# Optimization experiments

Hardware: AMD Instinct MI355X
Metric: run time of the kernel (lower is better)

## Reference

```python
import jax, jax.numpy as jnp
import numpy as np
import math

N_TOKEN = (56, 135, 18, 87, 18, 25)
EMB_SIZES = (128, 256, 64, 512, 128, 128)
D_MODEL = 512; N_LAYER = 12; N_HEAD = 8; D_HEAD = 64; D_FF = 2048
B = 2; S = 512
EPS_ATTN = 1e-6; EPS_LN = 1e-5


def _pos_encoding(seq, d):
    pos = jnp.arange(seq, dtype=jnp.float32)[:, None]
    div = jnp.exp(jnp.arange(0, d, 2, dtype=jnp.float32) * (-math.log(10000.0) / d))
    pe = jnp.zeros((seq, d), dtype=jnp.float32)
    pe = pe.at[:, 0::2].set(jnp.sin(pos * div))
    pe = pe.at[:, 1::2].set(jnp.cos(pos * div))
    return pe


def _ln(x, g, b):
    m = x.mean(-1, keepdims=True)
    v = ((x - m) ** 2).mean(-1, keepdims=True)
    return (x - m) * jax.lax.rsqrt(v + EPS_LN) * g + b


def setup_inputs():
    key = jax.random.key(0)
    ks = iter(jax.random.split(key, 128))
    def w(shape, s=0.02):
        return jax.random.normal(next(ks), shape, dtype=jnp.float32) * s
    inp = {}
    inp["x"] = jax.random.randint(next(ks), (B, S, 6), 0, min(N_TOKEN)).astype(jnp.int32)
    emb_names = ["emb_tempo", "emb_chord", "emb_barbeat", "emb_pitch", "emb_duration", "emb_velocity"]
    for n, v, e in zip(emb_names, N_TOKEN, EMB_SIZES):
        inp[n] = w((v, e), 1.0)
    inp["in_w"] = w((sum(EMB_SIZES), D_MODEL)); inp["in_b"] = jnp.zeros((D_MODEL,), jnp.float32)
    L = N_LAYER
    for nm, shp in [("Wq", (L, D_MODEL, D_MODEL)), ("Wk", (L, D_MODEL, D_MODEL)), ("Wv", (L, D_MODEL, D_MODEL)), ("Wo", (L, D_MODEL, D_MODEL)), ("W1", (L, D_MODEL, D_FF)), ("W2", (L, D_FF, D_MODEL))]:
        inp[nm] = w(shp)
    for nm, shp in [("bq", (L, D_MODEL)), ("bk", (L, D_MODEL)), ("bv", (L, D_MODEL)), ("bo", (L, D_MODEL)), ("bf1", (L, D_FF)), ("bf2", (L, D_MODEL)), ("b1n", (L, D_MODEL)), ("b2n", (L, D_MODEL))]:
        inp[nm] = jnp.zeros(shp, jnp.float32)
    inp["g1"] = jnp.ones((L, D_MODEL), jnp.float32); inp["g2"] = jnp.ones((L, D_MODEL), jnp.float32)
    inp["gf"] = jnp.ones((D_MODEL,), jnp.float32); inp["bfn"] = jnp.zeros((D_MODEL,), jnp.float32)
    for i, v in enumerate(N_TOKEN):
        inp[f"pw{i}"] = w((D_MODEL, v)); inp[f"pb{i}"] = jnp.zeros((v,), jnp.float32)
        inp[f"vw{i}"] = w((v, 1)); inp[f"vb{i}"] = jnp.zeros((1,), jnp.float32)
    return inp


def _layer(h, p):
    (wq, bq_, wk, bk_, wv, bv_, wo, bo_, g1_, b1_, g2_, b2_, w1, bf1_, w2, bf2_) = p
    # causal-linear attention (fast-transformers), feature map elu(x)+1
    q = (h @ wq + bq_).reshape(B, S, N_HEAD, D_HEAD)
    k = (h @ wk + bk_).reshape(B, S, N_HEAD, D_HEAD)
    v = (h @ wv + bv_).reshape(B, S, N_HEAD, D_HEAD)
    Q = jax.nn.elu(q) + 1.0
    K = jax.nn.elu(k) + 1.0
    kv = jnp.cumsum(jnp.einsum('bshd,bshm->bshdm', K, v), axis=1)  # causal prefix KV state
    num = jnp.einsum('bshd,bshdm->bshm', Q, kv)
    z = 1.0 / (jnp.einsum('bshd,bshd->bsh', Q, jnp.cumsum(K, axis=1)) + EPS_ATTN)
    a = (num * z[..., None]).reshape(B, S, D_MODEL) @ wo + bo_
    # fast-transformers TransformerEncoderLayer: post-norm residuals, exact GELU FFN
    h2 = _ln(h + a, g1_, b1_)
    y = jax.nn.gelu(h2 @ w1 + bf1_, approximate=False) @ w2 + bf2_
    return _ln(h2 + y, g2_, b2_), None


def reference(x, emb_tempo, emb_chord, emb_barbeat, emb_pitch, emb_duration, emb_velocity, in_w, in_b, Wq, bq, Wk, bk, Wv, bv, Wo, bo, g1, b1n, g2, b2n, W1, bf1, W2, bf2, gf, bfn, pw0, pb0, vw0, vb0, pw1, pb1, vw1, vb1, pw2, pb2, vw2, vb2, pw3, pb3, vw3, vb3, pw4, pb4, vw4, vb4, pw5, pb5, vw5, vb5):
    tables = [emb_tempo, emb_chord, emb_barbeat, emb_pitch, emb_duration, emb_velocity]
    embs = [tables[i][x[..., i]] * math.sqrt(EMB_SIZES[i]) for i in range(6)]
    h = jnp.concatenate(embs, axis=-1) @ in_w + in_b
    h = h + _pos_encoding(S, D_MODEL)
    h, _ = jax.lax.scan(jax.checkpoint(_layer), h, (Wq, bq, Wk, bk, Wv, bv, Wo, bo, g1, b1n, g2, b2n, W1, bf1, W2, bf2))
    h = _ln(h, gf, bfn)
    heads = [(pw0, pb0, vw0, vb0), (pw1, pb1, vw1, vb1), (pw2, pb2, vw2, vb2), (pw3, pb3, vw3, vb3), (pw4, pb4, vw4, vb4), (pw5, pb5, vw5, vb5)]
    total = 0.0
    for pw, pb, vw, vb in heads:
        total = total + jnp.mean((h @ pw + pb) @ vw + vb, axis=1)  # [B,1]
    return total / 6.0
```

## Files before the change

kernel.cpp:

```cpp
#include <hip/hip_runtime.h>
#include <math.h>

typedef _Float16 f16;
typedef _Float16 f16x8 __attribute__((ext_vector_type(8)));
typedef float f32x4 __attribute__((ext_vector_type(4)));

#define TOK 1024
#define DM  512
#define SEQ 512
#define NB  2
#define CHUNK 32
#define NCH (SEQ/CHUNK)

__global__ __launch_bounds__(256) void embed_gather(
    const int* __restrict__ x,
    const float* __restrict__ t0, const float* __restrict__ t1,
    const float* __restrict__ t2, const float* __restrict__ t3,
    const float* __restrict__ t4, const float* __restrict__ t5,
    f16* __restrict__ E) {
  int t = blockIdx.x;
  int tid = threadIdx.x;
  const int* xb = x + t * 6;
  for (int c = tid; c < 1216; c += 256) {
    float val;
    if (c < 128)       val = t0[xb[0]*128 + c]        * 11.313708498984761f;
    else if (c < 384)  val = t1[xb[1]*256 + (c-128)]  * 16.0f;
    else if (c < 448)  val = t2[xb[2]*64  + (c-384)]  * 8.0f;
    else if (c < 960)  val = t3[xb[3]*512 + (c-448)]  * 22.627416997969522f;
    else if (c < 1088) val = t4[xb[4]*128 + (c-960)]  * 11.313708498984761f;
    else               val = t5[xb[5]*128 + (c-1088)] * 11.313708498984761f;
    E[(size_t)t*1216 + c] = (f16)val;
  }
}

__global__ __launch_bounds__(256) void transp_convert(
    const float* __restrict__ in, f16* __restrict__ out,
    int K, int N, size_t instride, size_t outstride) {
  int lz = blockIdx.z;
  const float* I = in + (size_t)lz * instride;
  f16* O = out + (size_t)lz * outstride;
  __shared__ float tile[32][33];
  int k0 = blockIdx.x * 32, n0 = blockIdx.y * 32;
  int tid = threadIdx.x;
  int cr = tid >> 5, cc = tid & 31;
#pragma unroll
  for (int p = 0; p < 4; ++p)
    tile[cr + p*8][cc] = I[(size_t)(k0 + cr + p*8) * N + n0 + cc];
  __syncthreads();
#pragma unroll
  for (int p = 0; p < 4; ++p)
    O[(size_t)(n0 + cr + p*8) * K + k0 + cc] = (f16)tile[cc][cr + p*8];
}

__global__ __launch_bounds__(256) void transp_convert_qkvo(
    const float* __restrict__ Wq, const float* __restrict__ Wk,
    const float* __restrict__ Wv, const float* __restrict__ Wo,
    f16* __restrict__ qkvw, f16* __restrict__ wot) {
  int z = blockIdx.z;
  int lz = z >> 2, m = z & 3;
  const float* I = ((m == 0) ? Wq : (m == 1) ? Wk : (m == 2) ? Wv : Wo)
                   + (size_t)lz * 262144;
  f16* O = (m < 3) ? qkvw + (size_t)lz * 786432 + (size_t)m * 262144
                   : wot + (size_t)lz * 262144;
  __shared__ float tile[32][33];
  int k0 = blockIdx.x * 32, n0 = blockIdx.y * 32;
  int tid = threadIdx.x;
  int cr = tid >> 5, cc = tid & 31;
#pragma unroll
  for (int p = 0; p < 4; ++p)
    tile[cr + p*8][cc] = I[(size_t)(k0 + cr + p*8) * 512 + n0 + cc];
  __syncthreads();
#pragma unroll
  for (int p = 0; p < 4; ++p)
    O[(size_t)(n0 + cr + p*8) * 512 + k0 + cc] = (f16)tile[cc][cr + p*8];
}

template<int E>
__global__ __launch_bounds__(256) void mfma_gemm(
    const f16* __restrict__ A, const f16* __restrict__ Bt,
    const float* __restrict__ b0, const float* __restrict__ b1,
    const float* __restrict__ b2,
    float* __restrict__ o0, float* __restrict__ o1, float* __restrict__ o2,
    int M, int K, int N) {
  __shared__ f16 As[64][72];
  __shared__ f16 Bs[64][72];
  const int tid = threadIdx.x;
  const int m0 = blockIdx.x * 64, n0 = blockIdx.y * 64;
  const int w = tid >> 6, l = tid & 63;
  const int wr = w >> 1, wc = w & 1;
  const int g = l >> 4, r = l & 15;
  const int lr = tid >> 2, lc = (tid & 3) * 8;
  f32x4 acc[2][2] = {};
  const f16* Ap = A + (size_t)(m0 + lr) * K + lc;
  const f16* Bp = Bt + (size_t)(n0 + lr) * K + lc;
  for (int k0 = 0; k0 < K; k0 += 64) {
    *(f16x8*)&As[lr][lc]      = *(const f16x8*)(Ap + k0);
    *(f16x8*)&As[lr][lc + 32] = *(const f16x8*)(Ap + k0 + 32);
    *(f16x8*)&Bs[lr][lc]      = *(const f16x8*)(Bp + k0);
    *(f16x8*)&Bs[lr][lc + 32] = *(const f16x8*)(Bp + k0 + 32);
    __syncthreads();
#pragma unroll
    for (int kk = 0; kk < 2; ++kk) {
      f16x8 a0  = *(const f16x8*)&As[wr*32 + r][kk*32 + g*8];
      f16x8 a1  = *(const f16x8*)&As[wr*32 + 16 + r][kk*32 + g*8];
      f16x8 bv0 = *(const f16x8*)&Bs[wc*32 + r][kk*32 + g*8];
      f16x8 bv1 = *(const f16x8*)&Bs[wc*32 + 16 + r][kk*32 + g*8];
      acc[0][0] = __builtin_amdgcn_mfma_f32_16x16x32_f16(a0, bv0, acc[0][0], 0, 0, 0);
      acc[0][1] = __builtin_amdgcn_mfma_f32_16x16x32_f16(a0, bv1, acc[0][1], 0, 0, 0);
      acc[1][0] = __builtin_amdgcn_mfma_f32_16x16x32_f16(a1, bv0, acc[1][0], 0, 0, 0);
      acc[1][1] = __builtin_amdgcn_mfma_f32_16x16x32_f16(a1, bv1, acc[1][1], 0, 0, 0);
    }
    __syncthreads();
  }
#pragma unroll
  for (int m = 0; m < 2; ++m) {
    int row = m0 + wr*32 + m*16 + g*4;
#pragma unroll
    for (int n = 0; n < 2; ++n) {
      int col = n0 + wc*32 + n*16 + r;
      float pediv = 0.0f;
      if (E == 3) pediv = __expf((float)(col >> 1) * (-0.035977892070386504f));
#pragma unroll
      for (int i = 0; i < 4; ++i) {
        float v = acc[m][n][i];
        if (E == 2) {
          int which = col >> 9;
          int lc2 = col & 511;
          const float* bb = (which == 0) ? b0 : (which == 1) ? b1 : b2;
          float* oo = (which == 0) ? o0 : (which == 1) ? o1 : o2;
          v += bb[lc2];
          if (which < 2) v = (v > 0.0f) ? v + 1.0f : __expf(v);
          oo[(size_t)(row + i) * 512 + lc2] = v;
        } else if (E == 1) {
          v += b0[col];
          v = 0.5f * v * (1.0f + erff(v * 0.70710678118654752f));
          ((f16*)o0)[(size_t)(row + i) * N + col] = (f16)v;
        } else if (E == 3) {
          v += b0[col];
          float ang = (float)((row + i) & (SEQ-1)) * pediv;
          v += (col & 1) ? cosf(ang) : sinf(ang);
          o0[(size_t)(row + i) * N + col] = v;
          ((f16*)o1)[(size_t)(row + i) * N + col] = (f16)v;
        } else {
          v += b0[col];
          o0[(size_t)(row + i) * N + col] = v;
        }
      }
    }
  }
}

__global__ __launch_bounds__(256) void attn_chunk_sums(
    const float* __restrict__ Kg, const float* __restrict__ Vg,
    float* __restrict__ kvst, float* __restrict__ ksum) {
  int ch = blockIdx.x, bh = blockIdx.y;
  int b = bh >> 3, h = bh & 7;
  __shared__ float Ks[CHUNK][65], Vs[CHUNK][65];
  int tid = threadIdx.x;
  const float* Kbase = Kg + ((size_t)(b*SEQ + ch*CHUNK))*DM + h*64;
  const float* Vbase = Vg + ((size_t)(b*SEQ + ch*CHUNK))*DM + h*64;
#pragma unroll
  for (int l = 0; l < CHUNK*64/256; ++l) {
    int e = tid + l*256;
    int r = e >> 6, c = e & 63;
    Ks[r][c] = Kbase[(size_t)r*DM + c];
    Vs[r][c] = Vbase[(size_t)r*DM + c];
  }
  __syncthreads();
  int d = tid >> 2, m0 = (tid & 3) * 16;
  float acc[16] = {};
  for (int s = 0; s < CHUNK; ++s) {
    float kd = Ks[s][d];
#pragma unroll
    for (int j = 0; j < 16; ++j) acc[j] += kd * Vs[s][m0+j];
  }
  float* dst = kvst + (((size_t)(bh*NCH + ch)*64 + d)*64) + m0;
#pragma unroll
  for (int j4 = 0; j4 < 4; ++j4)
    *(float4*)(dst + j4*4) = make_float4(acc[j4*4], acc[j4*4+1], acc[j4*4+2], acc[j4*4+3]);
  if (tid < 64) {
    float s = 0;
    for (int r = 0; r < CHUNK; ++r) s += Ks[r][tid];
    ksum[(size_t)(bh*NCH + ch)*64 + tid] = s;
  }
}

__global__ __launch_bounds__(256) void attn_scan_par(
    float* __restrict__ kvst, float* __restrict__ ksum) {
  int slice = blockIdx.x;
  int bh = blockIdx.y;
  int tid = threadIdx.x;
  if (slice < 16) {
    size_t base = (size_t)bh*NCH*4096 + slice*256 + tid;
    float run = 0.0f;
    for (int ch = 0; ch < NCH; ++ch) {
      size_t idx = base + (size_t)ch*4096;
      float t = kvst[idx];
      kvst[idx] = run;
      run += t;
    }
  } else if (tid < 64) {
    size_t base = (size_t)bh*NCH*64 + tid;
    float run = 0.0f;
    for (int ch = 0; ch < NCH; ++ch) {
      size_t idx = base + (size_t)ch*64;
      float t = ksum[idx];
      ksum[idx] = run;
      run += t;
    }
  }
}

__global__ __launch_bounds__(256) void attn_chunk_out(
    const float* __restrict__ Qg, const float* __restrict__ Kg,
    const float* __restrict__ Vg, const float* __restrict__ kvst,
    const float* __restrict__ ksum, f16* __restrict__ O) {
  int ch = blockIdx.x, bh = blockIdx.y;
  int b = bh >> 3, h = bh & 7;
  __shared__ float Qs[CHUNK][65], Ks[CHUNK][65], Vs[CHUNK][65];
  __shared__ float kvp[64][65];
  __shared__ float Sl[CHUNK][CHUNK+1];
  __shared__ float ksp[64];
  __shared__ float den[CHUNK];
  int tid = threadIdx.x;
  const float* Qbase = Qg + ((size_t)(b*SEQ + ch*CHUNK))*DM + h*64;
  const float* Kbase = Kg + ((size_t)(b*SEQ + ch*CHUNK))*DM + h*64;
  const float* Vbase = Vg + ((size_t)(b*SEQ + ch*CHUNK))*DM + h*64;
#pragma unroll
  for (int ld = 0; ld < CHUNK*64/256; ++ld) {
    int e = tid + ld*256;
    int rr = e >> 6, cc = e & 63;
    Qs[rr][cc] = Qbase[(size_t)rr*DM + cc];
    Ks[rr][cc] = Kbase[(size_t)rr*DM + cc];
    Vs[rr][cc] = Vbase[(size_t)rr*DM + cc];
  }
  {
    const float* src = kvst + (size_t)(bh*NCH + ch)*4096;
#pragma unroll
    for (int ld = 0; ld < 16; ++ld) {
      int e = tid + ld*256;
      kvp[e >> 6][e & 63] = src[e];
    }
  }
  if (tid < 64) ksp[tid] = ksum[(size_t)(bh*NCH + ch)*64 + tid];
  __syncthreads();
#pragma unroll
  for (int ld = 0; ld < 4; ++ld) {
    int e = tid + ld*256;
    int i = e >> 5, j = e & 31;
    float s = 0;
    for (int d2 = 0; d2 < 64; ++d2) s += Qs[i][d2] * Ks[j][d2];
    Sl[i][j] = s;
  }
  __syncthreads();
  if (tid < CHUNK) {
    int i = tid;
    float dsum = 0;
    for (int d2 = 0; d2 < 64; ++d2) dsum += Qs[i][d2] * ksp[d2];
    for (int j = 0; j <= i; ++j) dsum += Sl[i][j];
    den[i] = 1.0f / (dsum + 1e-6f);
  }
  __syncthreads();
  int row = tid >> 3, m0 = (tid & 7) * 8;
  float acc[8] = {};
  for (int d2 = 0; d2 < 64; ++d2) {
    float qd = Qs[row][d2];
#pragma unroll
    for (int j = 0; j < 8; ++j) acc[j] += qd * kvp[d2][m0+j];
  }
  for (int j2 = 0; j2 <= row; ++j2) {
    float sv = Sl[row][j2];
#pragma unroll
    for (int j = 0; j < 8; ++j) acc[j] += sv * Vs[j2][m0+j];
  }
  float zi = den[row];
  f16* dst = O + ((size_t)(b*SEQ + ch*CHUNK + row))*DM + h*64 + m0;
#pragma unroll
  for (int j = 0; j < 8; ++j) dst[j] = (f16)(acc[j] * zi);
}

__global__ __launch_bounds__(256) void resid_ln(
    const float* __restrict__ x, const float* __restrict__ r,
    const float* __restrict__ g, const float* __restrict__ bb,
    float* __restrict__ out, f16* __restrict__ out16) {
  int t = blockIdx.x;
  int tid = threadIdx.x;
  __shared__ float red[256];
  const float* xb = x + (size_t)t*DM;
  float v0 = xb[tid];
  float v1 = xb[tid+256];
  if (r) {
    const float* rb = r + (size_t)t*DM;
    v0 += rb[tid];
    v1 += rb[tid+256];
  }
  red[tid] = v0 + v1;
  __syncthreads();
  for (int o = 128; o > 0; o >>= 1) {
    if (tid < o) red[tid] += red[tid+o];
    __syncthreads();
  }
  float mean = red[0] * (1.0f/512.0f);
  __syncthreads();
  float d0 = v0 - mean, d1 = v1 - mean;
  red[tid] = d0*d0 + d1*d1;
  __syncthreads();
  for (int o = 128; o > 0; o >>= 1) {
    if (tid < o) red[tid] += red[tid+o];
    __syncthreads();
  }
  float rs = rsqrtf(red[0] * (1.0f/512.0f) + 1e-5f);
  float r0 = d0*rs*g[tid]     + bb[tid];
  float r1 = d1*rs*g[tid+256] + bb[tid+256];
  out[(size_t)t*DM + tid]     = r0;
  out[(size_t)t*DM + tid+256] = r1;
  if (out16) {
    out16[(size_t)t*DM + tid]     = (f16)r0;
    out16[(size_t)t*DM + tid+256] = (f16)r1;
  }
}

struct HeadPtrs {
  const float* pw[6]; const float* pb[6];
  const float* vw[6]; const float* vb[6];
};

__global__ __launch_bounds__(64) void head_u_par(HeadPtrs hp, float* __restrict__ U,
                                                 float* __restrict__ Cc) {
  const int vsz[6] = {56, 135, 18, 87, 18, 25};
  const int off[6] = {0, 56, 191, 209, 296, 314};
  int d = blockIdx.x;
  int tid = threadIdx.x;
  float acc = 0.0f;
  for (int jj = tid; jj < 339; jj += 64) {
    int i;
    if (jj < 191) i = (jj < 56) ? 0 : 1;
    else if (jj < 296) i = (jj < 209) ? 2 : 3;
    else i = (jj < 314) ? 4 : 5;
    int j = jj - off[i];
    float wv = (d < 512) ? hp.pw[i][(size_t)d * vsz[i] + j] : hp.pb[i][j];
    acc += wv * hp.vw[i][j];
  }
#pragma unroll
  for (int s = 32; s > 0; s >>= 1) acc += __shfl_down(acc, s);
  if (tid == 0) {
    if (d < 512) U[d] = acc;
    else {
      for (int i = 0; i < 6; ++i) acc += hp.vb[i][0];
      Cc[0] = acc;
    }
  }
}

__global__ __launch_bounds__(512) void final_out(
    const float* __restrict__ hf, const float* __restrict__ U,
    const float* __restrict__ Cc, float* __restrict__ out) {
  int b = blockIdx.x;
  int d = threadIdx.x;
  __shared__ float red[512];
  float cs = 0;
  const float* hb = hf + (size_t)b*SEQ*DM + d;
  for (int s = 0; s < SEQ; ++s) cs += hb[(size_t)s*DM];
  red[d] = cs * U[d];
  __syncthreads();
  for (int o = 256; o > 0; o >>= 1) {
    if (d < o) red[d] += red[d+o];
    __syncthreads();
  }
  if (d == 0) out[b] = (red[0] * (1.0f/512.0f) + Cc[0]) * (1.0f/6.0f);
}

extern "C" void kernel_launch(void* const* d_in, const int* in_sizes, int n_in,
                              void* d_out, int out_size, void* d_ws, size_t ws_size,
                              hipStream_t stream) {
  const int*   x    = (const int*)d_in[0];
  const float* T0   = (const float*)d_in[1];
  const float* T1   = (const float*)d_in[2];
  const float* T2   = (const float*)d_in[3];
  const float* T3   = (const float*)d_in[4];
  const float* T4   = (const float*)d_in[5];
  const float* T5   = (const float*)d_in[6];
  const float* in_w = (const float*)d_in[7];
  const float* in_b = (const float*)d_in[8];
  const float* Wq   = (const float*)d_in[9];
  const float* Wk   = (const float*)d_in[10];
  const float* Wv   = (const float*)d_in[11];
  const float* Wo   = (const float*)d_in[12];
  const float* W1   = (const float*)d_in[13];
  const float* W2   = (const float*)d_in[14];
  const float* bq   = (const float*)d_in[15];
  const float* bk   = (const float*)d_in[16];
  const float* bv   = (const float*)d_in[17];
  const float* bo   = (const float*)d_in[18];
  const float* bf1  = (const float*)d_in[19];
  const float* bf2  = (const float*)d_in[20];
  const float* b1n  = (const float*)d_in[21];
  const float* b2n  = (const float*)d_in[22];
  const float* g1   = (const float*)d_in[23];
  const float* g2   = (const float*)d_in[24];
  const float* gf   = (const float*)d_in[25];
  const float* bfn  = (const float*)d_in[26];
  HeadPtrs hp;
  for (int i = 0; i < 6; ++i) {
    hp.pw[i] = (const float*)d_in[27 + i*4];
    hp.pb[i] = (const float*)d_in[28 + i*4];
    hp.vw[i] = (const float*)d_in[29 + i*4];
    hp.vb[i] = (const float*)d_in[30 + i*4];
  }

  float* ws   = (float*)d_ws;
  float* h    = ws;
  float* q    = h    + 524288;
  float* k    = q    + 524288;
  float* v    = k    + 524288;
  float* a2   = v    + 524288;
  float* h2   = a2   + 524288;
  float* y    = h2   + 524288;
  float* kvst = y    + 524288;
  float* ksum = kvst + 1048576;
  float* U    = ksum + 16384;
  float* Cc   = U    + 512;
  f16* E16    = (f16*)(Cc + 16);
  f16* hf16   = E16   + 1245184;
  f16* h2f16  = hf16  + 524288;
  f16* attn16 = h2f16 + 524288;
  f16* ff16   = attn16+ 524288;
  f16* in_wt  = ff16  + 2097152;
  f16* qkvw   = in_wt + 623616;
  f16* wot    = qkvw  + 9437184;
  f16* w1t    = wot   + 3145728;
  f16* w2t    = w1t   + 12582912;

  transp_convert<<<dim3(38,16,1),  256, 0, stream>>>(in_w, in_wt, 1216, 512, 0, 0);
  transp_convert_qkvo<<<dim3(16,16,48), 256, 0, stream>>>(Wq, Wk, Wv, Wo, qkvw, wot);
  transp_convert<<<dim3(16,64,12), 256, 0, stream>>>(W1, w1t,  512, 2048, 1048576, 1048576);
  transp_convert<<<dim3(64,16,12), 256, 0, stream>>>(W2, w2t, 2048,  512, 1048576, 1048576);

  embed_gather<<<TOK, 256, 0, stream>>>(x, T0, T1, T2, T3, T4, T5, E16);
  mfma_gemm<3><<<dim3(16,8), 256, 0, stream>>>(E16, in_wt, in_b, nullptr, nullptr,
                                               h, (float*)hf16, nullptr, TOK, 1216, 512);

  for (int l = 0; l < 12; ++l) {
    mfma_gemm<2><<<dim3(16,24), 256, 0, stream>>>(hf16, qkvw + (size_t)l*786432,
        bq + l*512, bk + l*512, bv + l*512, q, k, v, TOK, 512, 1536);
    attn_chunk_sums<<<dim3(NCH,16), 256, 0, stream>>>(k, v, kvst, ksum);
    attn_scan_par<<<dim3(17,16), 256, 0, stream>>>(kvst, ksum);
    attn_chunk_out<<<dim3(NCH,16), 256, 0, stream>>>(q, k, v, kvst, ksum, attn16);
    mfma_gemm<0><<<dim3(16,8), 256, 0, stream>>>(attn16, wot + (size_t)l*262144,
        bo + l*512, nullptr, nullptr, a2, nullptr, nullptr, TOK, 512, 512);
    resid_ln<<<TOK, 256, 0, stream>>>(h, a2, g1 + l*512, b1n + l*512, h2, h2f16);
    mfma_gemm<1><<<dim3(16,32), 256, 0, stream>>>(h2f16, w1t + (size_t)l*1048576,
        bf1 + l*2048, nullptr, nullptr, (float*)ff16, nullptr, nullptr, TOK, 512, 2048);
    mfma_gemm<0><<<dim3(16,8), 256, 0, stream>>>(ff16, w2t + (size_t)l*1048576,
        bf2 + l*512, nullptr, nullptr, y, nullptr, nullptr, TOK, 2048, 512);
    resid_ln<<<TOK, 256, 0, stream>>>(h2, y, g2 + l*512, b2n + l*512, h, hf16);
  }

  resid_ln<<<TOK, 256, 0, stream>>>(h, nullptr, gf, bfn, h2, nullptr);
  head_u_par<<<513, 64, 0, stream>>>(hp, U, Cc);
  final_out<<<NB, 512, 0, stream>>>(h2, U, Cc, (float*)d_out);
}
```

Baseline: 1.524 ms.

## Split-K the N=512 GEMMs and reduce partials inside the residual LayerNorm

The output-projection and FFN down-projection GEMMs (N=512, only 128 blocks) now use a split-K kernel that launches 2 and 4 K-slices respectively, writing fp32 partials. The residual LayerNorm kernel sums those partials and adds the bias, fusing the split-K reduction and bias into an existing pass. This is meant to raise GPU occupancy on the small-grid GEMMs, at the cost of extra partial-buffer writes and reads to global memory.

```diff
diff --git a/kernel.cpp b/kernel.cpp
--- a/kernel.cpp
+++ b/kernel.cpp
@@ -141,11 +141,56 @@
           v += (col & 1) ? cosf(ang) : sinf(ang);
           o0[(size_t)(row + i) * N + col] = v;
           ((f16*)o1)[(size_t)(row + i) * N + col] = (f16)v;
-        } else {
-          v += b0[col];
-          o0[(size_t)(row + i) * N + col] = v;
         }
       }
+    }
+  }
+}
+
+__global__ __launch_bounds__(256) void mfma_gemm_sk(
+    const f16* __restrict__ A, const f16* __restrict__ Bt,
+    float* __restrict__ P, int M, int K, int N, int KS) {
+  __shared__ f16 As[64][72];
+  __shared__ f16 Bs[64][72];
+  const int tid = threadIdx.x;
+  const int m0 = blockIdx.x * 64, n0 = blockIdx.y * 64;
+  const int z = blockIdx.z;
+  const int w = tid >> 6, l = tid & 63;
+  const int wr = w >> 1, wc = w & 1;
+  const int g = l >> 4, r = l & 15;
+  const int lr = tid >> 2, lc = (tid & 3) * 8;
+  f32x4 acc[2][2] = {};
+  const f16* Ap = A + (size_t)(m0 + lr) * K + z*KS + lc;
+  const f16* Bp = Bt + (size_t)(n0 + lr) * K + z*KS + lc;
+  for (int k0 = 0; k0 < KS; k0 += 64) {
+    *(f16x8*)&As[lr][lc]      = *(const f16x8*)(Ap + k0);
+    *(f16x8*)&As[lr][lc + 32] = *(const f16x8*)(Ap + k0 + 32);
+    *(f16x8*)&Bs[lr][lc]      = *(const f16x8*)(Bp + k0);
+    *(f16x8*)&Bs[lr][lc + 32] = *(const f16x8*)(Bp + k0 + 32);
+    __syncthreads();
+#pragma unroll
+    for (int kk = 0; kk < 2; ++kk) {
+      f16x8 a0  = *(const f16x8*)&As[wr*32 + r][kk*32 + g*8];
+      f16x8 a1  = *(const f16x8*)&As[wr*32 + 16 + r][kk*32 + g*8];
+      f16x8 bv0 = *(const f16x8*)&Bs[wc*32 + r][kk*32 + g*8];
+      f16x8 bv1 = *(const f16x8*)&Bs[wc*32 + 16 + r][kk*32 + g*8];
+      acc[0][0] = __builtin_amdgcn_mfma_f32_16x16x32_f16(a0, bv0, acc[0][0], 0, 0, 0);
+      acc[0][1] = __builtin_amdgcn_mfma_f32_16x16x32_f16(a0, bv1, acc[0][1], 0, 0, 0);
+      acc[1][0] = __builtin_amdgcn_mfma_f32_16x16x32_f16(a1, bv0, acc[1][0], 0, 0, 0);
+      acc[1][1] = __builtin_amdgcn_mfma_f32_16x16x32_f16(a1, bv1, acc[1][1], 0, 0, 0);
+    }
+    __syncthreads();
+  }
+  float* Pz = P + (size_t)z * M * N;
+#pragma unroll
+  for (int m = 0; m < 2; ++m) {
+    int row = m0 + wr*32 + m*16 + g*4;
+#pragma unroll
+    for (int n = 0; n < 2; ++n) {
+      int col = n0 + wc*32 + n*16 + r;
+#pragma unroll
+      for (int i = 0; i < 4; ++i)
+        Pz[(size_t)(row + i) * N + col] = acc[m][n][i];
     }
   }
 }
@@ -279,8 +324,9 @@
   for (int j = 0; j < 8; ++j) dst[j] = (f16)(acc[j] * zi);
 }
 
-__global__ __launch_bounds__(256) void resid_ln(
-    const float* __restrict__ x, const float* __restrict__ r,
+__global__ __launch_bounds__(256) void resid_ln_red(
+    const float* __restrict__ x, const float* __restrict__ P, int S,
+    const float* __restrict__ bias,
     const float* __restrict__ g, const float* __restrict__ bb,
     float* __restrict__ out, f16* __restrict__ out16) {
   int t = blockIdx.x;
@@ -289,10 +335,14 @@
   const float* xb = x + (size_t)t*DM;
   float v0 = xb[tid];
   float v1 = xb[tid+256];
-  if (r) {
-    const float* rb = r + (size_t)t*DM;
-    v0 += rb[tid];
-    v1 += rb[tid+256];
+  if (P) {
+    for (int s = 0; s < S; ++s) {
+      const float* Ps = P + (size_t)s*TOK*DM + (size_t)t*DM;
+      v0 += Ps[tid];
+      v1 += Ps[tid+256];
+    }
+    v0 += bias[tid];
+    v1 += bias[tid+256];
   }
   red[tid] = v0 + v1;
   __syncthreads();
@@ -413,10 +463,10 @@
   float* q    = h    + 524288;
   float* k    = q    + 524288;
   float* v    = k    + 524288;
-  float* a2   = v    + 524288;
-  float* h2   = a2   + 524288;
-  float* y    = h2   + 524288;
-  float* kvst = y    + 524288;
+  float* h2   = v    + 524288;
+  float* Pa   = h2   + 524288;
+  float* Pb   = Pa   + 1048576;
+  float* kvst = Pb   + 2097152;
   float* ksum = kvst + 1048576;
   float* U    = ksum + 16384;
   float* Cc   = U    + 512;
@@ -446,17 +496,19 @@
     attn_chunk_sums<<<dim3(NCH,16), 256, 0, stream>>>(k, v, kvst, ksum);
     attn_scan_par<<<dim3(17,16), 256, 0, stream>>>(kvst, ksum);
     attn_chunk_out<<<dim3(NCH,16), 256, 0, stream>>>(q, k, v, kvst, ksum, attn16);
-    mfma_gemm<0><<<dim3(16,8), 256, 0, stream>>>(attn16, wot + (size_t)l*262144,
-        bo + l*512, nullptr, nullptr, a2, nullptr, nullptr, TOK, 512, 512);
-    resid_ln<<<TOK, 256, 0, stream>>>(h, a2, g1 + l*512, b1n + l*512, h2, h2f16);
+    mfma_gemm_sk<<<dim3(16,8,2), 256, 0, stream>>>(attn16, wot + (size_t)l*262144,
+        Pa, TOK, 512, 512, 256);
+    resid_ln_red<<<TOK, 256, 0, stream>>>(h, Pa, 2, bo + l*512,
+        g1 + l*512, b1n + l*512, h2, h2f16);
     mfma_gemm<1><<<dim3(16,32), 256, 0, stream>>>(h2f16, w1t + (size_t)l*1048576,
         bf1 + l*2048, nullptr, nullptr, (float*)ff16, nullptr, nullptr, TOK, 512, 2048);
-    mfma_gemm<0><<<dim3(16,8), 256, 0, stream>>>(ff16, w2t + (size_t)l*1048576,
-        bf2 + l*512, nullptr, nullptr, y, nullptr, nullptr, TOK, 2048, 512);
-    resid_ln<<<TOK, 256, 0, stream>>>(h2, y, g2 + l*512, b2n + l*512, h, hf16);
-  }
-
-  resid_ln<<<TOK, 256, 0, stream>>>(h, nullptr, gf, bfn, h2, nullptr);
+    mfma_gemm_sk<<<dim3(16,8,4), 256, 0, stream>>>(ff16, w2t + (size_t)l*1048576,
+        Pb, TOK, 2048, 512, 512);
+    resid_ln_red<<<TOK, 256, 0, stream>>>(h2, Pb, 4, bf2 + l*512,
+        g2 + l*512, b2n + l*512, h, hf16);
+  }
+
+  resid_ln_red<<<TOK, 256, 0, stream>>>(h, nullptr, 0, nullptr, gf, bfn, h2, nullptr);
   head_u_par<<<513, 64, 0, stream>>>(hp, U, Cc);
   final_out<<<NB, 512, 0, stream>>>(h2, U, Cc, (float*)d_out);
 }
```

Result: faster. 1.246 ms (-18.2%).
